# Performance work log

Measured on AMD Instinct MI355X. Metric: run time of the kernel, lower is better.

The kernel has to match this reference:

```python
import jax, jax.numpy as jnp
import numpy as np

# Faithful, vectorized JAX version of Warpformer.hour_aggregate from SQHyper/Warpformer.
# Original loops over time_split=range(new_l+1) building per-bin masks and doing
# max_pool1d / masked sums; here we collapse that into segment reductions keyed by
# bin = floor(event_time) (since bins are [i, i+1)).


def setup_inputs() -> dict:
    key = jax.random.key(0)
    k1, k2, k3 = jax.random.split(key, 3)
    B, K, L, D = 16, 32, 1024, 128
    NEW_L = 48
    h0 = jax.random.normal(k1, (B, K, L, D), dtype=jnp.float32)
    # event times uniformly spread over the [0, NEW_L) window
    event_time = jax.random.uniform(k2, (B, L), dtype=jnp.float32) * NEW_L
    non_pad_mask = (jax.random.uniform(k3, (B, K, L)) > 0.1).astype(jnp.float32)
    return {"h0": h0, "event_time": event_time, "non_pad_mask": non_pad_mask, "new_l": NEW_L}


def reference(h0, event_time, non_pad_mask, new_l):
    b, k, l, d = h0.shape
    ns = new_l + 1  # extra dummy segment for out-of-range times
    valid = (event_time >= 0) & (event_time < new_l)
    seg = jnp.where(valid, jnp.floor(event_time).astype(jnp.int32), new_l)  # [b,l]

    def per_batch(h, et, npm, s):
        # h: [k,l,d], et: [l], npm: [k,l], s: [l]
        h_lkd = jnp.transpose(h, (1, 0, 2))                                   # [l,k,d]
        segmax = jax.ops.segment_max(h_lkd, s, num_segments=ns)               # [ns,k,d]
        counts = jax.ops.segment_sum(jnp.ones_like(et), s, num_segments=ns)   # [ns]
        tsum = jax.ops.segment_sum(et, s, num_segments=ns)                    # [ns]
        msum = jax.ops.segment_sum(jnp.transpose(npm, (1, 0)), s, num_segments=ns)  # [ns,k]
        return segmax, counts, tsum, msum

    segmax, counts, tsum, msum = jax.vmap(per_batch)(h0, event_time, non_pad_mask, seg)
    segmax = segmax[:, :new_l]   # [b,new_l,k,d]
    counts = counts[:, :new_l]   # [b,new_l]
    tsum = tsum[:, :new_l]
    msum = msum[:, :new_l]       # [b,new_l,k]

    denom = jnp.maximum(counts, 1.0)
    # Original does max_pool1d over h0*mask: zeros participate whenever bin has < l members
    # (empty bins -> 0, partially-filled bins -> max(members, 0)).
    include_zero = counts < l
    new_h0 = jnp.where(include_zero[:, :, None, None], jnp.maximum(segmax, 0.0), segmax)
    new_h0 = jnp.transpose(new_h0, (0, 2, 1, 3))  # [b,k,new_l,d]

    new_event_time = jnp.broadcast_to((tsum / denom)[:, None, :], (b, k, new_l))
    new_pad_mask = jnp.transpose(msum, (0, 2, 1)) / denom[:, None, :]  # [b,k,new_l]

    almat = (seg[:, :, None] == jnp.arange(new_l)[None, None, :]).astype(h0.dtype)  # [b,l,new_l]
    almat = jnp.broadcast_to(almat[:, None], (b, k, l, new_l))
    return new_h0, new_event_time, new_pad_mask, almat
```

## Files before the change

kernel.cpp:

```cpp
#include <hip/hip_runtime.h>
#include <math.h>

constexpr int CB = 16, CK = 32, CL = 1024, CD = 128, CNL = 48;

constexpr size_t OUT_H0 = 0;
constexpr size_t OUT_ET = (size_t)CB * CNL * CK * CD;
constexpr size_t OUT_PM = OUT_ET + (size_t)CB * CK * CNL;
constexpr size_t OUT_AL = OUT_PM + (size_t)CB * CK * CNL;

__device__ __forceinline__ unsigned fmap(float f) {
    int i = __float_as_int(f);
    return (i >= 0) ? ((unsigned)i | 0x80000000u) : ~(unsigned)i;
}
__device__ __forceinline__ float funmap(unsigned u) {
    return (u & 0x80000000u) ? __int_as_float((int)(u & 0x7FFFFFFFu))
                             : __int_as_float(~(int)u);
}
#define FMAP_NEG_INF 0x007FFFFFu

__global__ __launch_bounds__(256) void seg_kernel(
    const float* __restrict__ et, int* __restrict__ seg,
    float* __restrict__ counts, float* __restrict__ tsum) {
    __shared__ float cnt_s[CNL];
    __shared__ float ts_s[CNL];
    const int b = blockIdx.x;
    const int t = threadIdx.x;
    if (t < CNL) { cnt_s[t] = 0.f; ts_s[t] = 0.f; }
    __syncthreads();
    for (int l = t; l < CL; l += 256) {
        float e = et[b * CL + l];
        bool valid = (e >= 0.f) && (e < (float)CNL);
        int s = valid ? (int)floorf(e) : CNL;
        seg[b * CL + l] = s;
        if (valid) {
            atomicAdd(&cnt_s[s], 1.f);
            atomicAdd(&ts_s[s], e);
        }
    }
    __syncthreads();
    if (t < CNL) {
        counts[b * CNL + t] = cnt_s[t];
        tsum[b * CNL + t] = ts_s[t];
    }
}

__global__ __launch_bounds__(512) void main_kernel(
    const float* __restrict__ h0, const float* __restrict__ npm,
    const int* __restrict__ seg, const float* __restrict__ counts,
    const float* __restrict__ tsum, float* __restrict__ out) {
    __shared__ unsigned acc[(CNL + 1) * CD];
    __shared__ float msum_s[CNL + 1];
    __shared__ int segl[CL];

    const int bk = blockIdx.x;
    const int b = bk >> 5;
    const int t = threadIdx.x;

    for (int c = t; c < (CNL + 1) * CD; c += 512) acc[c] = FMAP_NEG_INF;
    if (t < CNL + 1) msum_s[t] = 0.f;
    for (int l = t; l < CL; l += 512) segl[l] = seg[b * CL + l];
    __syncthreads();

    {
        const float2* nrow = (const float2*)(npm + (size_t)bk * CL);
        float2 v = nrow[t];
        int l2 = t * 2;
        atomicAdd(&msum_s[segl[l2 + 0]], v.x);
        atomicAdd(&msum_s[segl[l2 + 1]], v.y);
    }

    const float* hbase = h0 + (size_t)bk * CL * CD;
    const int rg = t >> 7;
    const int d = t & 127;
    const int base = rg * 256;
    for (int i = 0; i < 256; i += 4) {
        const int l0 = base + i;
        float v0 = hbase[(size_t)(l0 + 0) * CD + d];
        float v1 = hbase[(size_t)(l0 + 1) * CD + d];
        float v2 = hbase[(size_t)(l0 + 2) * CD + d];
        float v3 = hbase[(size_t)(l0 + 3) * CD + d];
        int s0 = segl[l0 + 0];
        int s1 = segl[l0 + 1];
        int s2 = segl[l0 + 2];
        int s3 = segl[l0 + 3];
        atomicMax(&acc[s0 * CD + d], fmap(v0));
        atomicMax(&acc[s1 * CD + d], fmap(v1));
        atomicMax(&acc[s2 * CD + d], fmap(v2));
        atomicMax(&acc[s3 * CD + d], fmap(v3));
    }
    __syncthreads();

    for (int c = t; c < CNL * CD; c += 512) {
        int s = c >> 7;
        float v = funmap(acc[c]);
        float cn = counts[b * CNL + s];
        if (cn < (float)CL) v = fmaxf(v, 0.f);
        out[OUT_H0 + (size_t)bk * CNL * CD + c] = v;
    }
    if (t < CNL) {
        float cn = counts[b * CNL + t];
        float den = fmaxf(cn, 1.f);
        out[OUT_ET + (size_t)bk * CNL + t] = tsum[b * CNL + t] / den;
        out[OUT_PM + (size_t)bk * CNL + t] = msum_s[t] / den;
    }
}

__global__ __launch_bounds__(256) void almat_kernel(
    const int* __restrict__ seg, float4* __restrict__ out) {
    const int total4 = CB * CK * CL * (CNL / 4);
    const int stride = gridDim.x * blockDim.x;
    for (int i = blockIdx.x * blockDim.x + threadIdx.x; i < total4; i += stride) {
        int row = i / 12;
        int c4 = i - row * 12;
        int l = row & (CL - 1);
        int b = row >> 15;
        int s = seg[(b << 10) + l];
        int c = c4 * 4;
        float4 v;
        v.x = (c + 0 == s) ? 1.f : 0.f;
        v.y = (c + 1 == s) ? 1.f : 0.f;
        v.z = (c + 2 == s) ? 1.f : 0.f;
        v.w = (c + 3 == s) ? 1.f : 0.f;
        out[i] = v;
    }
}

extern "C" void kernel_launch(void* const* d_in, const int* in_sizes, int n_in,
                              void* d_out, int out_size, void* d_ws, size_t ws_size,
                              hipStream_t stream) {
    (void)in_sizes; (void)n_in; (void)out_size; (void)ws_size;
    const float* h0  = (const float*)d_in[0];
    const float* et  = (const float*)d_in[1];
    const float* npm = (const float*)d_in[2];
    float* out = (float*)d_out;

    int* seg = (int*)d_ws;
    float* counts = (float*)((char*)d_ws + (size_t)CB * CL * sizeof(int));
    float* tsum = counts + CB * CNL;

    seg_kernel<<<CB, 256, 0, stream>>>(et, seg, counts, tsum);
    main_kernel<<<CB * CK, 512, 0, stream>>>(h0, npm, seg, counts, tsum, out);
    almat_kernel<<<4096, 256, 0, stream>>>(seg, (float4*)(out + OUT_AL));
}
```

Before: 408.8 us.

## Fuse segment, main and almat kernels into one with float4 loads and swizzled LDS

Merges the three kernels into a single per-(b,k) kernel. Each block recomputes segment ids, counts and time sums from event_time itself, which removes the workspace round-trip and two launches. The almat one-hot writes move into the same block using the shared segment table. The h0 scan now uses float4 loads with an XOR swizzle on the LDS accumulator to spread bank traffic. The cost is that the small per-batch segment and count work is repeated 32 times, once per k.

```diff
diff --git a/kernel.cpp b/kernel.cpp
--- a/kernel.cpp
+++ b/kernel.cpp
@@ -4,7 +4,7 @@
 constexpr int CB = 16, CK = 32, CL = 1024, CD = 128, CNL = 48;
 
 constexpr size_t OUT_H0 = 0;
-constexpr size_t OUT_ET = (size_t)CB * CNL * CK * CD;
+constexpr size_t OUT_ET = (size_t)CB * CK * CNL * CD;
 constexpr size_t OUT_PM = OUT_ET + (size_t)CB * CK * CNL;
 constexpr size_t OUT_AL = OUT_PM + (size_t)CB * CK * CNL;
 
@@ -18,38 +18,15 @@
 }
 #define FMAP_NEG_INF 0x007FFFFFu
 
-__global__ __launch_bounds__(256) void seg_kernel(
-    const float* __restrict__ et, int* __restrict__ seg,
-    float* __restrict__ counts, float* __restrict__ tsum) {
-    __shared__ float cnt_s[CNL];
-    __shared__ float ts_s[CNL];
-    const int b = blockIdx.x;
-    const int t = threadIdx.x;
-    if (t < CNL) { cnt_s[t] = 0.f; ts_s[t] = 0.f; }
-    __syncthreads();
-    for (int l = t; l < CL; l += 256) {
-        float e = et[b * CL + l];
-        bool valid = (e >= 0.f) && (e < (float)CNL);
-        int s = valid ? (int)floorf(e) : CNL;
-        seg[b * CL + l] = s;
-        if (valid) {
-            atomicAdd(&cnt_s[s], 1.f);
-            atomicAdd(&ts_s[s], e);
-        }
-    }
-    __syncthreads();
-    if (t < CNL) {
-        counts[b * CNL + t] = cnt_s[t];
-        tsum[b * CNL + t] = ts_s[t];
-    }
-}
+__device__ __forceinline__ int swz(int d) { return d ^ (d >> 5); }
 
-__global__ __launch_bounds__(512) void main_kernel(
-    const float* __restrict__ h0, const float* __restrict__ npm,
-    const int* __restrict__ seg, const float* __restrict__ counts,
-    const float* __restrict__ tsum, float* __restrict__ out) {
+__global__ __launch_bounds__(512) void fused_kernel(
+    const float* __restrict__ h0, const float* __restrict__ et,
+    const float* __restrict__ npm, float* __restrict__ out) {
     __shared__ unsigned acc[(CNL + 1) * CD];
-    __shared__ float msum_s[CNL + 1];
+    __shared__ float cnt_s[CNL + 1];
+    __shared__ float ts_s[CNL + 1];
+    __shared__ float ms_s[CNL + 1];
     __shared__ int segl[CL];
 
     const int bk = blockIdx.x;
@@ -57,88 +34,85 @@
     const int t = threadIdx.x;
 
     for (int c = t; c < (CNL + 1) * CD; c += 512) acc[c] = FMAP_NEG_INF;
-    if (t < CNL + 1) msum_s[t] = 0.f;
-    for (int l = t; l < CL; l += 512) segl[l] = seg[b * CL + l];
+    if (t < CNL + 1) { cnt_s[t] = 0.f; ts_s[t] = 0.f; ms_s[t] = 0.f; }
     __syncthreads();
 
     {
-        const float2* nrow = (const float2*)(npm + (size_t)bk * CL);
-        float2 v = nrow[t];
-        int l2 = t * 2;
-        atomicAdd(&msum_s[segl[l2 + 0]], v.x);
-        atomicAdd(&msum_s[segl[l2 + 1]], v.y);
-    }
-
-    const float* hbase = h0 + (size_t)bk * CL * CD;
-    const int rg = t >> 7;
-    const int d = t & 127;
-    const int base = rg * 256;
-    for (int i = 0; i < 256; i += 4) {
-        const int l0 = base + i;
-        float v0 = hbase[(size_t)(l0 + 0) * CD + d];
-        float v1 = hbase[(size_t)(l0 + 1) * CD + d];
-        float v2 = hbase[(size_t)(l0 + 2) * CD + d];
-        float v3 = hbase[(size_t)(l0 + 3) * CD + d];
-        int s0 = segl[l0 + 0];
-        int s1 = segl[l0 + 1];
-        int s2 = segl[l0 + 2];
-        int s3 = segl[l0 + 3];
-        atomicMax(&acc[s0 * CD + d], fmap(v0));
-        atomicMax(&acc[s1 * CD + d], fmap(v1));
-        atomicMax(&acc[s2 * CD + d], fmap(v2));
-        atomicMax(&acc[s3 * CD + d], fmap(v3));
+        const float2 e2 = ((const float2*)(et + b * CL))[t];
+        const float2 m2 = ((const float2*)(npm + (size_t)bk * CL))[t];
+        const int l0 = 2 * t;
+        bool va = (e2.x >= 0.f) && (e2.x < (float)CNL);
+        bool vb = (e2.y >= 0.f) && (e2.y < (float)CNL);
+        int sa = va ? (int)e2.x : CNL;
+        int sb = vb ? (int)e2.y : CNL;
+        segl[l0] = sa;
+        segl[l0 + 1] = sb;
+        if (va) { atomicAdd(&cnt_s[sa], 1.f); atomicAdd(&ts_s[sa], e2.x); }
+        if (vb) { atomicAdd(&cnt_s[sb], 1.f); atomicAdd(&ts_s[sb], e2.y); }
+        atomicAdd(&ms_s[sa], m2.x);
+        atomicAdd(&ms_s[sb], m2.y);
     }
     __syncthreads();
 
+    const float* hb = h0 + (size_t)bk * CL * CD;
+    const int rlane = t >> 5;
+    const int d4 = (t & 31) * 4;
+    const int a0 = swz(d4 + 0);
+    const int a1 = swz(d4 + 1);
+    const int a2 = swz(d4 + 2);
+    const int a3 = swz(d4 + 3);
+#pragma unroll 4
+    for (int step = 0; step < 64; ++step) {
+        const int r = step * 16 + rlane;
+        const float4 v = *(const float4*)(hb + (size_t)r * CD + d4);
+        const int s = segl[r];
+        unsigned* arow = &acc[s * CD];
+        atomicMax(arow + a0, fmap(v.x));
+        atomicMax(arow + a1, fmap(v.y));
+        atomicMax(arow + a2, fmap(v.z));
+        atomicMax(arow + a3, fmap(v.w));
+    }
+    __syncthreads();
+
+    float* oh = out + OUT_H0 + (size_t)bk * CNL * CD;
     for (int c = t; c < CNL * CD; c += 512) {
-        int s = c >> 7;
-        float v = funmap(acc[c]);
-        float cn = counts[b * CNL + s];
-        if (cn < (float)CL) v = fmaxf(v, 0.f);
-        out[OUT_H0 + (size_t)bk * CNL * CD + c] = v;
+        const int s = c >> 7;
+        const int d = c & 127;
+        float v = funmap(acc[s * CD + swz(d)]);
+        if (cnt_s[s] < (float)CL) v = fmaxf(v, 0.f);
+        oh[c] = v;
     }
     if (t < CNL) {
-        float cn = counts[b * CNL + t];
-        float den = fmaxf(cn, 1.f);
-        out[OUT_ET + (size_t)bk * CNL + t] = tsum[b * CNL + t] / den;
-        out[OUT_PM + (size_t)bk * CNL + t] = msum_s[t] / den;
+        const float den = fmaxf(cnt_s[t], 1.f);
+        out[OUT_ET + (size_t)bk * CNL + t] = ts_s[t] / den;
+        out[OUT_PM + (size_t)bk * CNL + t] = ms_s[t] / den;
     }
-}
 
-__global__ __launch_bounds__(256) void almat_kernel(
-    const int* __restrict__ seg, float4* __restrict__ out) {
-    const int total4 = CB * CK * CL * (CNL / 4);
-    const int stride = gridDim.x * blockDim.x;
-    for (int i = blockIdx.x * blockDim.x + threadIdx.x; i < total4; i += stride) {
-        int row = i / 12;
-        int c4 = i - row * 12;
-        int l = row & (CL - 1);
-        int b = row >> 15;
-        int s = seg[(b << 10) + l];
-        int c = c4 * 4;
+    float4* oa = (float4*)(out + OUT_AL + (size_t)bk * CL * CNL);
+#pragma unroll
+    for (int i = 0; i < 24; ++i) {
+        const int idx = t + i * 512;
+        const int row = idx / 12;
+        const int c4 = idx - row * 12;
+        const int s = segl[row];
+        const int c = c4 * 4;
         float4 v;
         v.x = (c + 0 == s) ? 1.f : 0.f;
         v.y = (c + 1 == s) ? 1.f : 0.f;
         v.z = (c + 2 == s) ? 1.f : 0.f;
         v.w = (c + 3 == s) ? 1.f : 0.f;
-        out[i] = v;
+        oa[idx] = v;
     }
 }
 
 extern "C" void kernel_launch(void* const* d_in, const int* in_sizes, int n_in,
                               void* d_out, int out_size, void* d_ws, size_t ws_size,
                               hipStream_t stream) {
-    (void)in_sizes; (void)n_in; (void)out_size; (void)ws_size;
+    (void)in_sizes; (void)n_in; (void)out_size; (void)d_ws; (void)ws_size;
     const float* h0  = (const float*)d_in[0];
     const float* et  = (const float*)d_in[1];
     const float* npm = (const float*)d_in[2];
     float* out = (float*)d_out;
 
-    int* seg = (int*)d_ws;
-    float* counts = (float*)((char*)d_ws + (size_t)CB * CL * sizeof(int));
-    float* tsum = counts + CB * CNL;
-
-    seg_kernel<<<CB, 256, 0, stream>>>(et, seg, counts, tsum);
-    main_kernel<<<CB * CK, 512, 0, stream>>>(h0, npm, seg, counts, tsum, out);
-    almat_kernel<<<4096, 256, 0, stream>>>(seg, (float4*)(out + OUT_AL));
+    fused_kernel<<<CB * CK, 512, 0, stream>>>(h0, et, npm, out);
 }
```

New measurement: 410.3 us. Within noise of the previous version (+0.4%).
